# Performance work log

Measured on AMD Instinct MI355X. Metric: run time of the kernel, lower is better.

The kernel has to match this reference:

```python
import jax, jax.numpy as jnp
import numpy as np

H = 8          # num_heads
T = 2          # num_edge_types
NEG_SLOPE = 0.2


def _edge_softmax(scores, dst, num_nodes):
    # softmax over incoming edges of each destination node, per head
    m = jax.ops.segment_max(scores, dst, num_segments=num_nodes)  # [N,H]
    e = jnp.exp(scores - m[dst])                                   # [E,H]
    s = jax.ops.segment_sum(e, dst, num_segments=num_nodes)        # [N,H]
    return e / s[dst]


def setup_inputs() -> dict:
    key = jax.random.key(0)
    ks = jax.random.split(key, 8)
    N, D, E = 50000, 128, 800000
    return {
        "x": jax.random.normal(ks[0], (N, D), dtype=jnp.float32),
        "w_u": jax.random.normal(ks[1], (H * T, D), dtype=jnp.float32) * (1.0 / np.sqrt(D)),
        "b_u": jax.random.normal(ks[2], (H * T,), dtype=jnp.float32) * 0.01,
        "w_v": jax.random.normal(ks[3], (H * T, D), dtype=jnp.float32) * (1.0 / np.sqrt(D)),
        "src_e0": jax.random.randint(ks[4], (E,), 0, N, dtype=jnp.int32),
        "dst_e0": jax.random.randint(ks[5], (E,), 0, N, dtype=jnp.int32),
        "src_e1": jax.random.randint(ks[6], (E,), 0, N, dtype=jnp.int32),
        "dst_e1": jax.random.randint(ks[7], (E,), 0, N, dtype=jnp.int32),
    }


def reference(x, w_u, b_u, w_v, src_e0, dst_e0, src_e1, dst_e1):
    N, D = x.shape
    head_dim = D // H
    scores_u = x @ w_u.T + b_u   # [N, H*T]
    scores_v = x @ w_v.T         # [N, H*T]
    xh = x.reshape(N, head_dim, H)  # matches torch reshape(-1, head_dim, num_heads)
    outs = [x]  # sep=True
    for t, (src, dst) in enumerate([(src_e0, dst_e0), (src_e1, dst_e1)]):
        u = scores_u[:, t * H:(t + 1) * H]
        v = scores_v[:, t * H:(t + 1) * H]
        s = u[src] + v[dst]                         # u_add_v -> [E,H]
        s = jnp.where(s >= 0, s, NEG_SLOPE * s)     # LeakyReLU(0.2)
        p = _edge_softmax(s, dst, N)                # [E,H]
        msg = xh[src] * p[:, None, :]               # u_mul_e -> [E,head_dim,H]
        agg = jax.ops.segment_sum(msg, dst, num_segments=N)  # [N,head_dim,H]
        outs.append(agg.reshape(N, D))
    return jnp.concatenate(outs, axis=-1)  # [N, D*(1+T)]
```

## Files before the change

### kernel.cpp

```cpp
#include <hip/hip_runtime.h>

#define NEG_SLOPE 0.2f
#define RSHIFT 6
#define RW     64
#define MAXNR  800
#define CHUNKP 8192

__device__ __forceinline__ ushort f2bf(float f) {
    union { float f; unsigned u; } c; c.f = f;
    unsigned u = c.u;
    return (ushort)((u + 0x7fffu + ((u >> 16) & 1u)) >> 16);
}
__device__ __forceinline__ float bflo(unsigned u) { return __uint_as_float(u << 16); }
__device__ __forceinline__ float bfhi(unsigned u) { return __uint_as_float(u & 0xffff0000u); }

__global__ __launch_bounds__(256) void mega_kernel(
    const float* __restrict__ x, const float* __restrict__ wu,
    const float* __restrict__ bu, const float* __restrict__ wv,
    const int* __restrict__ s0, const int* __restrict__ d0,
    const int* __restrict__ s1, const int* __restrict__ d1,
    float* __restrict__ out, ushort* __restrict__ xbf,
    float* __restrict__ su, float* __restrict__ sv,
    int* __restrict__ gcur, unsigned* __restrict__ pairs,
    int N, int E, int nr, int cap, int convBlocks, int scoreBlocks, int ppset)
{
    __shared__ float wlds[32 * 129];
    int* smi = (int*)wlds;
    int tid = threadIdx.x;
    int bid = blockIdx.x;

    if (bid < 2 * ppset) {
        int pb = bid;
        int t = pb / ppset, c = pb % ppset;
        const int* ss = t ? s1 : s0;
        const int* dd = t ? d1 : d0;
        int beg = c * CHUNKP, end = min(E, beg + CHUNKP);
        int* lcnt = smi; int* gb = smi + MAXNR; int* lrun = smi + 2 * MAXNR;
        for (int i = tid; i < nr; i += 256) lcnt[i] = 0;
        __syncthreads();
        for (int e = beg + tid; e < end; e += 256)
            atomicAdd(&lcnt[dd[e] >> RSHIFT], 1);
        __syncthreads();
        for (int i = tid; i < nr; i += 256) {
            gb[i] = atomicAdd(&gcur[t * nr + i], lcnt[i]);
            lrun[i] = 0;
        }
        __syncthreads();
        unsigned* pt = pairs + (size_t)t * nr * cap;
        for (int e = beg + tid; e < end; e += 256) {
            int dst = dd[e], src = ss[e];
            int rr = dst >> RSHIFT;
            int pos = atomicAdd(&lrun[rr], 1);
            pt[(size_t)rr * cap + gb[rr] + pos] = ((unsigned)dst << 16) | (unsigned)src;
        }
        return;
    }
    if (bid < 2 * ppset + convBlocks) {
        int i = (bid - 2 * ppset) * 256 + tid;
        if (i < N * 32) {
            float4 v = ((const float4*)x)[i];
            int n = i >> 5, q = i & 31;
            ((float4*)out)[(size_t)n * 96 + q] = v;
            ushort4 b;
            b.x = f2bf(v.x); b.y = f2bf(v.y); b.z = f2bf(v.z); b.w = f2bf(v.w);
            *(ushort4*)(xbf + (size_t)i * 4) = b;
        }
        return;
    }
    for (int i = tid; i < 4096; i += 256) {
        int o = i >> 7, k = i & 127;
        wlds[o * 129 + k] = (o < 16) ? wu[i] : wv[i - 2048];
    }
    __syncthreads();
    int o = tid & 15;
    int n = (bid - 2 * ppset - convBlocks) * 16 + (tid >> 4);
    if (n >= N) return;
    const float4* xr4 = (const float4*)(x + (size_t)n * 128);
    const float* wur = wlds + o * 129;
    const float* wvr = wlds + (16 + o) * 129;
    float au = 0.f, av = 0.f;
#pragma unroll
    for (int kk = 0; kk < 32; ++kk) {
        float4 xv = xr4[kk];
        int k = kk * 4;
        au = fmaf(xv.x, wur[k],     au);  av = fmaf(xv.x, wvr[k],     av);
        au = fmaf(xv.y, wur[k + 1], au);  av = fmaf(xv.y, wvr[k + 1], av);
        au = fmaf(xv.z, wur[k + 2], au);  av = fmaf(xv.z, wvr[k + 2], av);
        au = fmaf(xv.w, wur[k + 3], au);  av = fmaf(xv.w, wvr[k + 3], av);
    }
    su[n * 16 + o] = au + bu[o];
    sv[n * 16 + o] = av;
}

__global__ __launch_bounds__(256, 8) void buildagg_kernel(
    const ushort* __restrict__ xbf, const float* __restrict__ su,
    const float* __restrict__ sv, const int* __restrict__ gcur,
    const unsigned* __restrict__ pairs, float* __restrict__ out,
    int N, int E, int nr, int cap)
{
    __shared__ ushort srcs[1408];
    __shared__ int offl[65];
    __shared__ int cursor[64];
    __shared__ __align__(16) float ev4[4][512];
    int r = blockIdx.x, t = blockIdx.y, tid = threadIdx.x;
    int m = gcur[t * nr + r];
    if (m > cap) m = cap;
    const unsigned* p = pairs + ((size_t)t * nr + r) * cap;

    if (tid < 64) cursor[tid] = 0;
    __syncthreads();
    for (int i = tid; i < m; i += 256)
        atomicAdd(&cursor[(p[i] >> 16) & (RW - 1)], 1);
    __syncthreads();
    if (tid < 64) {
        int v = cursor[tid];
        int incl = v;
#pragma unroll
        for (int d = 1; d < 64; d <<= 1) {
            int o = __shfl(incl, tid - d);
            if (tid >= d) incl += o;
        }
        offl[tid + 1] = incl;
        if (tid == 0) offl[0] = 0;
        cursor[tid] = incl - v;
    }
    __syncthreads();
    for (int i = tid; i < m; i += 256) {
        unsigned v = p[i];
        int pos = atomicAdd(&cursor[(v >> 16) & (RW - 1)], 1);
        srcs[pos] = (ushort)(v & 0xffffu);
    }
    __syncthreads();

    int wid = tid >> 6, lane = tid & 63;
    int h = lane & 7, e8 = lane >> 3;
    int g2 = lane >> 4, q16 = lane & 15;
    int j0 = q16 * 8;
    float* ev = ev4[wid];
    for (int ln = wid; ln < RW; ln += 4) {
        int n = (r << RSHIFT) + ln;
        if (n >= N) break;
        int beg = offl[ln], end = offl[ln + 1];
        float vh = sv[n * 16 + t * 8 + h];
        float a0 = 0.f, a1 = 0.f, a2 = 0.f, a3 = 0.f;
        float a4 = 0.f, a5 = 0.f, a6 = 0.f, a7 = 0.f;
        float l = 0.f;
        for (int cbeg = beg; cbeg < end; cbeg += 64) {
            int cnt = min(end - cbeg, 64);
            int gmax = (cnt + 7) >> 3;
            for (int g = 0; g < gmax; g += 2) {
                int ea = g * 8 + e8, eb = ea + 8;
                int sa = srcs[cbeg + ((ea < cnt) ? ea : 0)];
                int sb = srcs[cbeg + ((eb < cnt) ? eb : 0)];
                float fa = su[sa * 16 + t * 8 + h];
                float fb = su[sb * 16 + t * 8 + h];
                float sca = fa + vh;
                float scb = fb + vh;
                sca = (sca >= 0.f) ? sca : NEG_SLOPE * sca;
                scb = (scb >= 0.f) ? scb : NEG_SLOPE * scb;
                float eea = (ea < cnt) ? __expf(sca) : 0.f;
                float eeb = (eb < cnt) ? __expf(scb) : 0.f;
                l += eea;
                l += eeb;
                ev[ea * 8 + h] = eea;
                ev[eb * 8 + h] = eeb;
            }
            int quads = (cnt + 3) >> 2;
            for (int i4 = 0; i4 < quads; i4 += 2) {
                int e0 = (i4 << 2) + g2, e1 = e0 + 4;
                int sA = srcs[cbeg + ((e0 < cnt) ? e0 : 0)];
                int sB = srcs[cbeg + ((e1 < cnt) ? e1 : 0)];
                uint4 uA = *(const uint4*)(xbf + (size_t)sA * 128 + j0);
                uint4 uB = *(const uint4*)(xbf + (size_t)sB * 128 + j0);
                float4 pA0 = *(const float4*)(ev + e0 * 8);
                float4 pA1 = *(const float4*)(ev + e0 * 8 + 4);
                float4 pB0 = *(const float4*)(ev + e1 * 8);
                float4 pB1 = *(const float4*)(ev + e1 * 8 + 4);
                a0 = fmaf(bflo(uA.x), pA0.x, a0);
                a1 = fmaf(bfhi(uA.x), pA0.y, a1);
                a2 = fmaf(bflo(uA.y), pA0.z, a2);
                a3 = fmaf(bfhi(uA.y), pA0.w, a3);
                a4 = fmaf(bflo(uA.z), pA1.x, a4);
                a5 = fmaf(bfhi(uA.z), pA1.y, a5);
                a6 = fmaf(bflo(uA.w), pA1.z, a6);
                a7 = fmaf(bfhi(uA.w), pA1.w, a7);
                a0 = fmaf(bflo(uB.x), pB0.x, a0);
                a1 = fmaf(bfhi(uB.x), pB0.y, a1);
                a2 = fmaf(bflo(uB.y), pB0.z, a2);
                a3 = fmaf(bfhi(uB.y), pB0.w, a3);
                a4 = fmaf(bflo(uB.z), pB1.x, a4);
                a5 = fmaf(bfhi(uB.z), pB1.y, a5);
                a6 = fmaf(bflo(uB.w), pB1.z, a6);
                a7 = fmaf(bfhi(uB.w), pB1.w, a7);
            }
        }
        l += __shfl_xor(l, 8);
        l += __shfl_xor(l, 16);
        l += __shfl_xor(l, 32);
        float invl = (l > 0.f) ? (1.f / l) : 0.f;
        a0 += __shfl_xor(a0, 16); a0 += __shfl_xor(a0, 32);
        a1 += __shfl_xor(a1, 16); a1 += __shfl_xor(a1, 32);
        a2 += __shfl_xor(a2, 16); a2 += __shfl_xor(a2, 32);
        a3 += __shfl_xor(a3, 16); a3 += __shfl_xor(a3, 32);
        a4 += __shfl_xor(a4, 16); a4 += __shfl_xor(a4, 32);
        a5 += __shfl_xor(a5, 16); a5 += __shfl_xor(a5, 32);
        a6 += __shfl_xor(a6, 16); a6 += __shfl_xor(a6, 32);
        a7 += __shfl_xor(a7, 16); a7 += __shfl_xor(a7, 32);
        float ih0 = __shfl(invl, 0);
        float ih1 = __shfl(invl, 1);
        float ih2 = __shfl(invl, 2);
        float ih3 = __shfl(invl, 3);
        float ih4 = __shfl(invl, 4);
        float ih5 = __shfl(invl, 5);
        float ih6 = __shfl(invl, 6);
        float ih7 = __shfl(invl, 7);
        if (g2 == 0) {
            float* op = out + (size_t)n * 384 + 128 + (size_t)t * 128 + j0;
            *(float4*)op       = make_float4(a0 * ih0, a1 * ih1, a2 * ih2, a3 * ih3);
            *(float4*)(op + 4) = make_float4(a4 * ih4, a5 * ih5, a6 * ih6, a7 * ih7);
        }
    }
}

extern "C" void kernel_launch(void* const* d_in, const int* in_sizes, int n_in,
                              void* d_out, int out_size, void* d_ws, size_t ws_size,
                              hipStream_t stream)
{
    const float* x  = (const float*)d_in[0];
    const float* wu = (const float*)d_in[1];
    const float* bu = (const float*)d_in[2];
    const float* wv = (const float*)d_in[3];
    const int* s0 = (const int*)d_in[4];
    const int* d0 = (const int*)d_in[5];
    const int* s1 = (const int*)d_in[6];
    const int* d1 = (const int*)d_in[7];
    float* out = (float*)d_out;
    int N = in_sizes[0] / 128;
    int E = in_sizes[4];

    int nr = ((N - 1) >> RSHIFT) + 1;
    long long mean = (long long)RW * E / N;
    int cap = (int)(mean + mean / 4 + 64);

    char* ws = (char*)d_ws;
    size_t o = 0;
    auto alloc = [&](size_t bytes) -> void* {
        void* p = ws + o;
        o = (o + bytes + 255) & ~(size_t)255;
        return p;
    };
    float* su       = (float*)alloc((size_t)N * 16 * 4);
    float* sv       = (float*)alloc((size_t)N * 16 * 4);
    int* gcur       = (int*)alloc((size_t)2 * nr * 4);
    unsigned* pairs = (unsigned*)alloc((size_t)2 * nr * cap * 4);
    ushort* xbf     = (ushort*)alloc((size_t)N * 128 * 2);

    int convBlocks  = (N * 32 + 255) / 256;
    int scoreBlocks = (N + 15) / 16;
    int ppset       = (E + CHUNKP - 1) / CHUNKP;

    hipMemsetAsync(gcur, 0, (size_t)2 * nr * 4, stream);
    mega_kernel<<<convBlocks + scoreBlocks + 2 * ppset, 256, 0, stream>>>(
        x, wu, bu, wv, s0, d0, s1, d1, out, xbf, su, sv,
        gcur, pairs, N, E, nr, cap, convBlocks, scoreBlocks, ppset);
    buildagg_kernel<<<dim3(nr, 2), 256, 0, stream>>>(
        xbf, su, sv, gcur, pairs, out, N, E, nr, cap);
}
```

Measured before the change: 234.6 us.

## Fuse x conversion into score blocks and halve destination bucket width

The separate conversion blocks are folded into the score-projection blocks. Each block now loads its 16 rows of x once, writes the copy to out and to the bf16 buffer, and keeps the rows in LDS for the dot products, so x is no longer read from global memory twice. The destination bucket width also drops from 64 to 32 nodes, which doubles the number of aggregation blocks and shrinks their shared buffers. That gives more parallelism in the aggregation phase, at the cost of more partition buckets, more global atomics on the counters, and a different per-bucket capacity.

New measurement: 231.6 us. About the same (-1.3%).

```diff
diff --git a/kernel.cpp b/kernel.cpp
--- a/kernel.cpp
+++ b/kernel.cpp
@@ -1,9 +1,9 @@
 #include <hip/hip_runtime.h>
 
 #define NEG_SLOPE 0.2f
-#define RSHIFT 6
-#define RW     64
-#define MAXNR  800
+#define RSHIFT 5
+#define RW     32
+#define MAXNR  1600
 #define CHUNKP 8192
 
 __device__ __forceinline__ ushort f2bf(float f) {
@@ -22,10 +22,12 @@
     float* __restrict__ out, ushort* __restrict__ xbf,
     float* __restrict__ su, float* __restrict__ sv,
     int* __restrict__ gcur, unsigned* __restrict__ pairs,
-    int N, int E, int nr, int cap, int convBlocks, int scoreBlocks, int ppset)
+    int N, int E, int nr, int cap, int scoreBlocks, int ppset)
 {
-    __shared__ float wlds[32 * 129];
-    int* smi = (int*)wlds;
+    __shared__ __align__(16) float smemf[32 * 129 + 16 * 132];
+    int* smi = (int*)smemf;
+    float* wlds = smemf;
+    float* xtile = smemf + 32 * 129;
     int tid = threadIdx.x;
     int bid = blockIdx.x;
 
@@ -55,27 +57,32 @@
         }
         return;
     }
-    if (bid < 2 * ppset + convBlocks) {
-        int i = (bid - 2 * ppset) * 256 + tid;
-        if (i < N * 32) {
-            float4 v = ((const float4*)x)[i];
-            int n = i >> 5, q = i & 31;
+    int nb = bid - 2 * ppset;
+    int base = nb * 16;
+    for (int i = tid; i < 4096; i += 256) {
+        int o = i >> 7, k = i & 127;
+        wlds[o * 129 + k] = (o < 16) ? wu[i] : wv[i - 2048];
+    }
+    for (int i2 = tid; i2 < 512; i2 += 256) {
+        int I = nb * 512 + i2;
+        int nl = i2 >> 5, q = i2 & 31;
+        int n = base + nl;
+        float4 v = make_float4(0.f, 0.f, 0.f, 0.f);
+        if (n < N) {
+            v = ((const float4*)x)[I];
             ((float4*)out)[(size_t)n * 96 + q] = v;
             ushort4 b;
             b.x = f2bf(v.x); b.y = f2bf(v.y); b.z = f2bf(v.z); b.w = f2bf(v.w);
-            *(ushort4*)(xbf + (size_t)i * 4) = b;
-        }
-        return;
-    }
-    for (int i = tid; i < 4096; i += 256) {
-        int o = i >> 7, k = i & 127;
-        wlds[o * 129 + k] = (o < 16) ? wu[i] : wv[i - 2048];
+            *(ushort4*)(xbf + (size_t)I * 4) = b;
+        }
+        ((float4*)(xtile + nl * 132))[q] = v;
     }
     __syncthreads();
     int o = tid & 15;
-    int n = (bid - 2 * ppset - convBlocks) * 16 + (tid >> 4);
+    int nl = tid >> 4;
+    int n = base + nl;
     if (n >= N) return;
-    const float4* xr4 = (const float4*)(x + (size_t)n * 128);
+    const float4* xr4 = (const float4*)(xtile + nl * 132);
     const float* wur = wlds + o * 129;
     const float* wvr = wlds + (16 + o) * 129;
     float au = 0.f, av = 0.f;
@@ -98,25 +105,25 @@
     const unsigned* __restrict__ pairs, float* __restrict__ out,
     int N, int E, int nr, int cap)
 {
-    __shared__ ushort srcs[1408];
-    __shared__ int offl[65];
-    __shared__ int cursor[64];
+    __shared__ ushort srcs[768];
+    __shared__ int offl[33];
+    __shared__ int cursor[32];
     __shared__ __align__(16) float ev4[4][512];
     int r = blockIdx.x, t = blockIdx.y, tid = threadIdx.x;
     int m = gcur[t * nr + r];
     if (m > cap) m = cap;
     const unsigned* p = pairs + ((size_t)t * nr + r) * cap;
 
-    if (tid < 64) cursor[tid] = 0;
+    if (tid < 32) cursor[tid] = 0;
     __syncthreads();
     for (int i = tid; i < m; i += 256)
         atomicAdd(&cursor[(p[i] >> 16) & (RW - 1)], 1);
     __syncthreads();
-    if (tid < 64) {
+    if (tid < 32) {
         int v = cursor[tid];
         int incl = v;
 #pragma unroll
-        for (int d = 1; d < 64; d <<= 1) {
+        for (int d = 1; d < 32; d <<= 1) {
             int o = __shfl(incl, tid - d);
             if (tid >= d) incl += o;
         }
@@ -255,14 +262,13 @@
     unsigned* pairs = (unsigned*)alloc((size_t)2 * nr * cap * 4);
     ushort* xbf     = (ushort*)alloc((size_t)N * 128 * 2);
 
-    int convBlocks  = (N * 32 + 255) / 256;
     int scoreBlocks = (N + 15) / 16;
     int ppset       = (E + CHUNKP - 1) / CHUNKP;
 
     hipMemsetAsync(gcur, 0, (size_t)2 * nr * 4, stream);
-    mega_kernel<<<convBlocks + scoreBlocks + 2 * ppset, 256, 0, stream>>>(
+    mega_kernel<<<scoreBlocks + 2 * ppset, 256, 0, stream>>>(
         x, wu, bu, wv, s0, d0, s1, d1, out, xbf, su, sv,
-        gcur, pairs, N, E, nr, cap, convBlocks, scoreBlocks, ppset);
+        gcur, pairs, N, E, nr, cap, scoreBlocks, ppset);
     buildagg_kernel<<<dim3(nr, 2), 256, 0, stream>>>(
         xbf, su, sv, gcur, pairs, out, N, E, nr, cap);
 }
```
